# Kernel tuning notes

Measured on AMD Instinct MI355X. Metric: run time of the kernel, lower is better.

Reference implementation:

```python
import jax, jax.numpy as jnp
import numpy as np

N_NODES = 100000
N_EDGES = 3200000
F_IN = 512
F_OUT = 256


def setup_inputs() -> dict:
    key = jax.random.key(0)
    k1, k2, k3, k4, k5 = jax.random.split(key, 5)
    x = jax.random.normal(k1, (N_NODES, F_IN), dtype=jnp.float32)
    adj_rows = jax.random.randint(k2, (N_EDGES,), 0, N_NODES, dtype=jnp.int32)
    adj_cols = jax.random.randint(k3, (N_EDGES,), 0, N_NODES, dtype=jnp.int32)
    adj_vals = jax.random.uniform(k4, (N_EDGES,), dtype=jnp.float32)
    # glorot-uniform weight as in glorot_init
    init_range = np.sqrt(6.0 / (F_IN + F_OUT))
    weight = jax.random.uniform(k5, (F_IN, F_OUT), dtype=jnp.float32,
                                minval=-init_range, maxval=init_range)
    return {"x": x, "adj_rows": adj_rows, "adj_cols": adj_cols,
            "adj_vals": adj_vals, "weight": weight}


def reference(x, adj_rows, adj_cols, adj_vals, adj_rows_dummy=None, **_):
    raise NotImplementedError  # replaced below


def reference(x, adj_rows, adj_cols, adj_vals, weight):
    # dropout p=0.0 -> identity
    h = jnp.matmul(x, weight)                      # [N, Fout] dense GEMM
    # SpMM: out[r] = sum_e vals[e] * h[cols[e]] for rows[e]==r
    msgs = adj_vals[:, None] * h[adj_cols]         # [E, Fout] gather + scale
    out = jax.ops.segment_sum(msgs, adj_rows, num_segments=x.shape[0])
    return jax.nn.relu(out)
```

## Files before the change

kernel.cpp:

```cpp
#include <hip/hip_runtime.h>

#define F_IN 512
#define F_OUT 256
#define BM 128
#define BN 256
#define BK 64

#define RB_BITS 7
#define RPB 128
#define NBUCK 1024
#define NSUB 8
#define CAP_SUB 1024
#define LDSCAP 5120
#define CSTR 16

typedef __attribute__((ext_vector_type(8))) short bf16x8;
typedef __attribute__((ext_vector_type(4))) float f32x4;
typedef __attribute__((ext_vector_type(4))) int i32x4;

__device__ __forceinline__ ushort f2bf(float f) {
    union { float f; unsigned u; } c{f};
    unsigned r = (c.u + 0x7FFF + ((c.u >> 16) & 1)) >> 16;
    return (ushort)r;
}
__device__ __forceinline__ float bf2f(ushort b) {
    union { unsigned u; float f; } c{(unsigned)b << 16};
    return c.f;
}

__global__ __launch_bounds__(256) void conv_w(const float* __restrict__ w,
                                              ushort* __restrict__ wt) {
    int idx = blockIdx.x * 256 + threadIdx.x;
    int k = idx & (F_IN - 1);
    int n = idx >> 9;
    wt[(size_t)n * F_IN + k] = f2bf(w[(size_t)k * F_OUT + n]);
}

__global__ __launch_bounds__(512) void gemm_mfma(const float* __restrict__ x,
                                                 const ushort* __restrict__ wt,
                                                 ushort* __restrict__ h,
                                                 int n_nodes) {
    __shared__ short As[BM * BK];
    __shared__ short Bs[BN * BK];
    const int t = threadIdx.x;
    const int lane = t & 63;
    const int w = t >> 6;
    const int wm = w >> 2;
    const int wn = w & 3;
    const int row0 = blockIdx.x * BM;

    f32x4 acc[4][4] = {};

    const int arow = t >> 2;
    const int akq  = (t & 3) << 4;
    const bool avalid = (row0 + arow) < n_nodes;
    const float* xsrc = x + (size_t)(row0 + arow) * F_IN + akq;

    const int lrow = lane & 15;
    const int koff = (lane >> 4) << 3;

    f32x4 fA[4];
    bf16x8 fB[4];

    {
        if (avalid) {
            const f32x4* s4 = reinterpret_cast<const f32x4*>(xsrc);
            fA[0] = __builtin_nontemporal_load(s4 + 0);
            fA[1] = __builtin_nontemporal_load(s4 + 1);
            fA[2] = __builtin_nontemporal_load(s4 + 2);
            fA[3] = __builtin_nontemporal_load(s4 + 3);
        } else {
            fA[0] = 0.f; fA[1] = 0.f; fA[2] = 0.f; fA[3] = 0.f;
        }
#pragma unroll
        for (int p = 0; p < 4; ++p) {
            int cid = p * 512 + t;
            int n = cid >> 3;
            int j = cid & 7;
            fB[p] = *reinterpret_cast<const bf16x8*>(wt + (size_t)n * F_IN + j * 8);
        }
    }

    for (int k0 = 0; k0 < F_IN; k0 += BK) {
#pragma unroll
        for (int q = 0; q < 2; ++q) {
            bf16x8 v;
#pragma unroll
            for (int j = 0; j < 8; ++j) v[j] = (short)f2bf(fA[q * 2 + (j >> 2)][j & 3]);
            int kk = akq + q * 8;
            int idx = arow * BK + (kk ^ ((arow & 7) << 3));
            *reinterpret_cast<bf16x8*>(&As[idx]) = v;
        }
#pragma unroll
        for (int p = 0; p < 4; ++p) {
            int cid = p * 512 + t;
            int n = cid >> 3;
            int j = cid & 7;
            int idx = n * BK + ((j * 8) ^ ((n & 7) << 3));
            *reinterpret_cast<bf16x8*>(&Bs[idx]) = fB[p];
        }
        __syncthreads();

        if (k0 + BK < F_IN) {
            if (avalid) {
                const f32x4* s4 = reinterpret_cast<const f32x4*>(xsrc + k0 + BK);
                fA[0] = __builtin_nontemporal_load(s4 + 0);
                fA[1] = __builtin_nontemporal_load(s4 + 1);
                fA[2] = __builtin_nontemporal_load(s4 + 2);
                fA[3] = __builtin_nontemporal_load(s4 + 3);
            }
#pragma unroll
            for (int p = 0; p < 4; ++p) {
                int cid = p * 512 + t;
                int n = cid >> 3;
                int j = cid & 7;
                fB[p] = *reinterpret_cast<const bf16x8*>(wt + (size_t)n * F_IN + k0 + BK + j * 8);
            }
        }

#pragma unroll
        for (int kk = 0; kk < BK; kk += 32) {
            bf16x8 a[4], b[4];
#pragma unroll
            for (int m = 0; m < 4; ++m) {
                int r = wm * 64 + m * 16 + lrow;
                int idx = r * BK + ((kk + koff) ^ ((r & 7) << 3));
                a[m] = *reinterpret_cast<const bf16x8*>(&As[idx]);
            }
#pragma unroll
            for (int n = 0; n < 4; ++n) {
                int r = wn * 64 + n * 16 + lrow;
                int idx = r * BK + ((kk + koff) ^ ((r & 7) << 3));
                b[n] = *reinterpret_cast<const bf16x8*>(&Bs[idx]);
            }
#pragma unroll
            for (int m = 0; m < 4; ++m)
#pragma unroll
                for (int n = 0; n < 4; ++n)
                    acc[m][n] = __builtin_amdgcn_mfma_f32_16x16x32_bf16(a[m], b[n], acc[m][n], 0, 0, 0);
        }
        __syncthreads();
    }

    const int rbase = (lane >> 4) << 2;
#pragma unroll
    for (int m = 0; m < 4; ++m) {
#pragma unroll
        for (int r = 0; r < 4; ++r) {
            int orow = row0 + wm * 64 + m * 16 + rbase + r;
            if (orow < n_nodes) {
                ushort* dst = h + (size_t)orow * F_OUT + wn * 64 + lrow;
#pragma unroll
                for (int n = 0; n < 4; ++n) dst[n * 16] = f2bf(acc[m][n][r]);
            }
        }
    }
}

__global__ __launch_bounds__(256) void bucket_place(const int* __restrict__ rows,
                                                    const int* __restrict__ cols,
                                                    const float* __restrict__ vals,
                                                    int* __restrict__ bcur,
                                                    int2* __restrict__ edges,
                                                    int n_edges) {
    const int sub = blockIdx.x & (NSUB - 1);
    int base = (blockIdx.x * 256 + threadIdx.x) * 4;
    if (base >= n_edges) return;
    if (base + 3 < n_edges) {
        i32x4 r4 = __builtin_nontemporal_load(reinterpret_cast<const i32x4*>(rows + base));
        i32x4 c4 = __builtin_nontemporal_load(reinterpret_cast<const i32x4*>(cols + base));
        f32x4 v4 = __builtin_nontemporal_load(reinterpret_cast<const f32x4*>(vals + base));
#pragma unroll
        for (int j = 0; j < 4; ++j) {
            int r = r4[j];
            int bs = (r >> RB_BITS) * NSUB + sub;
            int p = atomicAdd(&bcur[bs * CSTR], 1);
            if (p < CAP_SUB)
                edges[(size_t)bs * CAP_SUB + p] =
                    make_int2(((r & (RPB - 1)) << 17) | c4[j], __float_as_int(v4[j]));
        }
    } else {
        for (int j = 0; j < 4 && base + j < n_edges; ++j) {
            int r = rows[base + j];
            int bs = (r >> RB_BITS) * NSUB + sub;
            int p = atomicAdd(&bcur[bs * CSTR], 1);
            if (p < CAP_SUB)
                edges[(size_t)bs * CAP_SUB + p] =
                    make_int2(((r & (RPB - 1)) << 17) | cols[base + j],
                              __float_as_int(vals[base + j]));
        }
    }
}

__global__ __launch_bounds__(256) void bucket_sort(const int* __restrict__ bcur,
                                                   int2* __restrict__ edges,
                                                   int* __restrict__ offs,
                                                   int* __restrict__ oend,
                                                   int n_nodes) {
    __shared__ int2 raw[LDSCAP];
    __shared__ int cnt[RPB];
    __shared__ int lcur[RPB];
    __shared__ int wtot;
    const int b = blockIdx.x;
    const int t = threadIdx.x;
    const size_t bbase = (size_t)b * NSUB * CAP_SUB;

    if (t < RPB) cnt[t] = 0;
    __syncthreads();

    int nraw = 0;
#pragma unroll
    for (int s = 0; s < NSUB; ++s) {
        int ns = bcur[(b * NSUB + s) * CSTR];
        if (ns > CAP_SUB) ns = CAP_SUB;
        int take = ns;
        if (nraw + take > LDSCAP) take = LDSCAP - nraw;
        for (int i = t; i < take; i += 256) {
            int2 e = edges[bbase + (size_t)s * CAP_SUB + i];
            raw[nraw + i] = e;
            atomicAdd(&cnt[e.x >> 17], 1);
        }
        nraw += take;
    }
    __syncthreads();

    int c = (t < RPB) ? cnt[t] : 0;
    int padded = (c + 7) & ~7;
    int x = padded;
#pragma unroll
    for (int d = 1; d < 64; d <<= 1) {
        int y = __shfl_up(x, d, 64);
        if ((t & 63) >= d) x += y;
    }
    if (t == 63) wtot = x;
    __syncthreads();
    if (t < RPB) {
        int mybase = x - padded + ((t >= 64) ? wtot : 0);
        lcur[t] = mybase;
        int gr = (b << RB_BITS) + t;
        if (gr < n_nodes) {
            offs[gr] = (int)bbase + mybase;
            oend[gr] = (int)bbase + mybase + padded;
        }
        for (int j = c; j < padded; ++j)
            edges[bbase + mybase + j] = make_int2(0, 0);
    }
    __syncthreads();

    for (int i = t; i < nraw; i += 256) {
        int2 e = raw[i];
        int r7 = e.x >> 17;
        int pos = atomicAdd(&lcur[r7], 1);
        edges[bbase + pos] = make_int2(e.x & 0x1FFFF, e.y);
    }
}

struct EB { i32x4 e0, e1, e2, e3; };
struct GB { ushort4 g0, g1, g2, g3, g4, g5, g6, g7; };

__device__ __forceinline__ void load_eb(EB& e, const int2* __restrict__ edges, int i) {
    const i32x4* ep = reinterpret_cast<const i32x4*>(edges + i);
    e.e0 = __builtin_nontemporal_load(ep + 0);
    e.e1 = __builtin_nontemporal_load(ep + 1);
    e.e2 = __builtin_nontemporal_load(ep + 2);
    e.e3 = __builtin_nontemporal_load(ep + 3);
}
__device__ __forceinline__ void issue_gb(GB& g, const EB& e, const ushort* __restrict__ hf) {
    g.g0 = *reinterpret_cast<const ushort4*>(hf + (size_t)e.e0[0] * F_OUT);
    g.g1 = *reinterpret_cast<const ushort4*>(hf + (size_t)e.e0[2] * F_OUT);
    g.g2 = *reinterpret_cast<const ushort4*>(hf + (size_t)e.e1[0] * F_OUT);
    g.g3 = *reinterpret_cast<const ushort4*>(hf + (size_t)e.e1[2] * F_OUT);
    g.g4 = *reinterpret_cast<const ushort4*>(hf + (size_t)e.e2[0] * F_OUT);
    g.g5 = *reinterpret_cast<const ushort4*>(hf + (size_t)e.e2[2] * F_OUT);
    g.g6 = *reinterpret_cast<const ushort4*>(hf + (size_t)e.e3[0] * F_OUT);
    g.g7 = *reinterpret_cast<const ushort4*>(hf + (size_t)e.e3[2] * F_OUT);
}
__device__ __forceinline__ void fma1(float* acc, float v, ushort4 g) {
    acc[0] = fmaf(v, bf2f(g.x), acc[0]);
    acc[1] = fmaf(v, bf2f(g.y), acc[1]);
    acc[2] = fmaf(v, bf2f(g.z), acc[2]);
    acc[3] = fmaf(v, bf2f(g.w), acc[3]);
}
__device__ __forceinline__ void fma_gb(float* acc, const EB& e, const GB& g) {
    fma1(acc, __int_as_float(e.e0[1]), g.g0);
    fma1(acc, __int_as_float(e.e0[3]), g.g1);
    fma1(acc, __int_as_float(e.e1[1]), g.g2);
    fma1(acc, __int_as_float(e.e1[3]), g.g3);
    fma1(acc, __int_as_float(e.e2[1]), g.g4);
    fma1(acc, __int_as_float(e.e2[3]), g.g5);
    fma1(acc, __int_as_float(e.e3[1]), g.g6);
    fma1(acc, __int_as_float(e.e3[3]), g.g7);
}

__global__ __launch_bounds__(256) void spmm_csr(const int* __restrict__ offs,
                                                const int* __restrict__ oend,
                                                const int2* __restrict__ edges,
                                                const ushort* __restrict__ h,
                                                float* __restrict__ out,
                                                int n_nodes) {
    const int row = (int)((blockIdx.x * blockDim.x + threadIdx.x) >> 6);
    if (row >= n_nodes) return;
    const int lane = threadIdx.x & 63;
    const int beg = offs[row];
    const int end = oend[row];
    const int nb = (end - beg) >> 3;

    float acc[4] = {0.f, 0.f, 0.f, 0.f};
    const ushort* hf = h + lane * 4;

    if (nb > 0) {
        EB ea, eb_;
        GB ga, gb;
        load_eb(ea, edges, beg);
        issue_gb(ga, ea, hf);
        int bi = 1;
        for (; bi + 1 < nb; bi += 2) {
            load_eb(eb_, edges, beg + bi * 8);
            issue_gb(gb, eb_, hf);
            fma_gb(acc, ea, ga);
            load_eb(ea, edges, beg + (bi + 1) * 8);
            issue_gb(ga, ea, hf);
            fma_gb(acc, eb_, gb);
        }
        if (bi < nb) {
            load_eb(eb_, edges, beg + bi * 8);
            issue_gb(gb, eb_, hf);
            fma_gb(acc, ea, ga);
            fma_gb(acc, eb_, gb);
        } else {
            fma_gb(acc, ea, ga);
        }
    }

    f32x4 o;
    o[0] = fmaxf(acc[0], 0.f);
    o[1] = fmaxf(acc[1], 0.f);
    o[2] = fmaxf(acc[2], 0.f);
    o[3] = fmaxf(acc[3], 0.f);
    __builtin_nontemporal_store(o, reinterpret_cast<f32x4*>(out + (size_t)row * F_OUT + lane * 4));
}

static inline size_t align_up(size_t v, size_t a) { return (v + a - 1) & ~(a - 1); }

extern "C" void kernel_launch(void* const* d_in, const int* in_sizes, int n_in,
                              void* d_out, int out_size, void* d_ws, size_t ws_size,
                              hipStream_t stream) {
    const float* x    = (const float*)d_in[0];
    const int*   rows = (const int*)d_in[1];
    const int*   cols = (const int*)d_in[2];
    const float* vals = (const float*)d_in[3];
    const float* w    = (const float*)d_in[4];
    float* out = (float*)d_out;

    const int n_nodes = in_sizes[0] / F_IN;
    const int n_edges = in_sizes[1];
    const int nbuck_used = (n_nodes + RPB - 1) >> RB_BITS;

    char* ws = (char*)d_ws;
    size_t off = 0;
    ushort* h   = (ushort*)(ws + off); off = align_up(off + (size_t)n_nodes * F_OUT * 2, 256);
    ushort* wt  = (ushort*)(ws + off); off = align_up(off + (size_t)F_OUT * F_IN * 2, 256);
    int2* edges = (int2*)(ws + off);   off = align_up(off + (size_t)NBUCK * NSUB * CAP_SUB * 8, 256);
    int* offs   = (int*)(ws + off);    off = align_up(off + (size_t)n_nodes * 4, 256);
    int* oend   = (int*)(ws + off);    off = align_up(off + (size_t)n_nodes * 4, 256);
    int* bcur   = (int*)(ws + off);    off = align_up(off + (size_t)NBUCK * NSUB * CSTR * 4, 256);
    (void)ws_size;

    conv_w<<<(F_IN * F_OUT) / 256, 256, 0, stream>>>(w, wt);

    gemm_mfma<<<(n_nodes + BM - 1) / BM, 512, 0, stream>>>(x, wt, h, n_nodes);

    hipMemsetAsync(bcur, 0, (size_t)NBUCK * NSUB * CSTR * 4, stream);
    bucket_place<<<(n_edges / 4 + 255) / 256, 256, 0, stream>>>(rows, cols, vals, bcur,
                                                                edges, n_edges);
    bucket_sort<<<nbuck_used, 256, 0, stream>>>(bcur, edges, offs, oend, n_nodes);

    spmm_csr<<<(n_nodes * 64 + 255) / 256, 256, 0, stream>>>(offs, oend, edges, h, out, n_nodes);
}
```

Baseline: 513.5 us.

## Fuse GEMM and edge bucketing into one launch; sub-sort edges by column

```diff
diff --git a/kernel.cpp b/kernel.cpp
--- a/kernel.cpp
+++ b/kernel.cpp
@@ -13,6 +13,7 @@
 #define CAP_SUB 1024
 #define LDSCAP 5120
 #define CSTR 16
+#define NBIN (RPB * 32)
 
 typedef __attribute__((ext_vector_type(8))) short bf16x8;
 typedef __attribute__((ext_vector_type(4))) float f32x4;
@@ -36,18 +37,61 @@
     wt[(size_t)n * F_IN + k] = f2bf(w[(size_t)k * F_OUT + n]);
 }
 
-__global__ __launch_bounds__(512) void gemm_mfma(const float* __restrict__ x,
-                                                 const ushort* __restrict__ wt,
-                                                 ushort* __restrict__ h,
-                                                 int n_nodes) {
+__global__ __launch_bounds__(512) void gemm_place(const float* __restrict__ x,
+                                                  const ushort* __restrict__ wt,
+                                                  ushort* __restrict__ h,
+                                                  int n_nodes,
+                                                  const int* __restrict__ rows,
+                                                  const int* __restrict__ cols,
+                                                  const float* __restrict__ vals,
+                                                  int* __restrict__ bcur,
+                                                  int2* __restrict__ edges,
+                                                  int n_edges,
+                                                  int ngemm) {
     __shared__ short As[BM * BK];
     __shared__ short Bs[BN * BK];
+    const int bid = blockIdx.x;
     const int t = threadIdx.x;
+
+    const bool is_gemm = (bid % 3 == 0) && (bid / 3 < ngemm);
+    if (!is_gemm) {
+        const int place_id = (bid < 3 * ngemm) ? (bid - bid / 3 - 1) : (bid - ngemm);
+        const int sub = bid & (NSUB - 1);
+        int base = (place_id * 512 + t) * 4;
+        if (base >= n_edges) return;
+        if (base + 3 < n_edges) {
+            i32x4 r4 = __builtin_nontemporal_load(reinterpret_cast<const i32x4*>(rows + base));
+            i32x4 c4 = __builtin_nontemporal_load(reinterpret_cast<const i32x4*>(cols + base));
+            f32x4 v4 = __builtin_nontemporal_load(reinterpret_cast<const f32x4*>(vals + base));
+#pragma unroll
+            for (int j = 0; j < 4; ++j) {
+                int r = r4[j];
+                int bs = (r >> RB_BITS) * NSUB + sub;
+                int p = atomicAdd(&bcur[bs * CSTR], 1);
+                if (p < CAP_SUB)
+                    edges[(size_t)bs * CAP_SUB + p] =
+                        make_int2(((r & (RPB - 1)) << 17) | c4[j], __float_as_int(v4[j]));
+            }
+        } else {
+            for (int j = 0; j < 4 && base + j < n_edges; ++j) {
+                int r = rows[base + j];
+                int bs = (r >> RB_BITS) * NSUB + sub;
+                int p = atomicAdd(&bcur[bs * CSTR], 1);
+                if (p < CAP_SUB)
+                    edges[(size_t)bs * CAP_SUB + p] =
+                        make_int2(((r & (RPB - 1)) << 17) | cols[base + j],
+                                  __float_as_int(vals[base + j]));
+            }
+        }
+        return;
+    }
+
+    const int gb = bid / 3;
     const int lane = t & 63;
     const int w = t >> 6;
     const int wm = w >> 2;
     const int wn = w & 3;
-    const int row0 = blockIdx.x * BM;
+    const int row0 = gb * BM;
 
     f32x4 acc[4][4] = {};
 
@@ -157,55 +201,19 @@
     }
 }
 
-__global__ __launch_bounds__(256) void bucket_place(const int* __restrict__ rows,
-                                                    const int* __restrict__ cols,
-                                                    const float* __restrict__ vals,
-                                                    int* __restrict__ bcur,
-                                                    int2* __restrict__ edges,
-                                                    int n_edges) {
-    const int sub = blockIdx.x & (NSUB - 1);
-    int base = (blockIdx.x * 256 + threadIdx.x) * 4;
-    if (base >= n_edges) return;
-    if (base + 3 < n_edges) {
-        i32x4 r4 = __builtin_nontemporal_load(reinterpret_cast<const i32x4*>(rows + base));
-        i32x4 c4 = __builtin_nontemporal_load(reinterpret_cast<const i32x4*>(cols + base));
-        f32x4 v4 = __builtin_nontemporal_load(reinterpret_cast<const f32x4*>(vals + base));
-#pragma unroll
-        for (int j = 0; j < 4; ++j) {
-            int r = r4[j];
-            int bs = (r >> RB_BITS) * NSUB + sub;
-            int p = atomicAdd(&bcur[bs * CSTR], 1);
-            if (p < CAP_SUB)
-                edges[(size_t)bs * CAP_SUB + p] =
-                    make_int2(((r & (RPB - 1)) << 17) | c4[j], __float_as_int(v4[j]));
-        }
-    } else {
-        for (int j = 0; j < 4 && base + j < n_edges; ++j) {
-            int r = rows[base + j];
-            int bs = (r >> RB_BITS) * NSUB + sub;
-            int p = atomicAdd(&bcur[bs * CSTR], 1);
-            if (p < CAP_SUB)
-                edges[(size_t)bs * CAP_SUB + p] =
-                    make_int2(((r & (RPB - 1)) << 17) | cols[base + j],
-                              __float_as_int(vals[base + j]));
-        }
-    }
-}
-
 __global__ __launch_bounds__(256) void bucket_sort(const int* __restrict__ bcur,
                                                    int2* __restrict__ edges,
                                                    int* __restrict__ offs,
                                                    int* __restrict__ oend,
                                                    int n_nodes) {
     __shared__ int2 raw[LDSCAP];
-    __shared__ int cnt[RPB];
-    __shared__ int lcur[RPB];
+    __shared__ int cnt[NBIN];
     __shared__ int wtot;
     const int b = blockIdx.x;
     const int t = threadIdx.x;
     const size_t bbase = (size_t)b * NSUB * CAP_SUB;
 
-    if (t < RPB) cnt[t] = 0;
+    for (int i = t; i < NBIN; i += 256) cnt[i] = 0;
     __syncthreads();
 
     int nraw = 0;
@@ -218,14 +226,19 @@
         for (int i = t; i < take; i += 256) {
             int2 e = edges[bbase + (size_t)s * CAP_SUB + i];
             raw[nraw + i] = e;
-            atomicAdd(&cnt[e.x >> 17], 1);
+            int key = ((e.x >> 17) << 5) | ((e.x & 0x1FFFF) >> 12);
+            atomicAdd(&cnt[key], 1);
         }
         nraw += take;
     }
     __syncthreads();
 
-    int c = (t < RPB) ? cnt[t] : 0;
-    int padded = (c + 7) & ~7;
+    int rowtot = 0;
+    if (t < RPB) {
+#pragma unroll
+        for (int j = 0; j < 32; ++j) rowtot += cnt[(t << 5) + j];
+    }
+    int padded = (rowtot + 7) & ~7;
     int x = padded;
 #pragma unroll
     for (int d = 1; d < 64; d <<= 1) {
@@ -235,22 +248,28 @@
     if (t == 63) wtot = x;
     __syncthreads();
     if (t < RPB) {
-        int mybase = x - padded + ((t >= 64) ? wtot : 0);
-        lcur[t] = mybase;
+        int rb = x - padded + ((t >= 64) ? wtot : 0);
         int gr = (b << RB_BITS) + t;
         if (gr < n_nodes) {
-            offs[gr] = (int)bbase + mybase;
-            oend[gr] = (int)bbase + mybase + padded;
-        }
-        for (int j = c; j < padded; ++j)
-            edges[bbase + mybase + j] = make_int2(0, 0);
+            offs[gr] = (int)bbase + rb;
+            oend[gr] = (int)bbase + rb + padded;
+        }
+        for (int j = rowtot; j < padded; ++j)
+            edges[bbase + rb + j] = make_int2(0, 0);
+        int run = rb;
+#pragma unroll
+        for (int j = 0; j < 32; ++j) {
+            int c2 = cnt[(t << 5) + j];
+            cnt[(t << 5) + j] = run;
+            run += c2;
+        }
     }
     __syncthreads();
 
     for (int i = t; i < nraw; i += 256) {
         int2 e = raw[i];
-        int r7 = e.x >> 17;
-        int pos = atomicAdd(&lcur[r7], 1);
+        int key = ((e.x >> 17) << 5) | ((e.x & 0x1FFFF) >> 12);
+        int pos = atomicAdd(&cnt[key], 1);
         edges[bbase + pos] = make_int2(e.x & 0x1FFFF, e.y);
     }
 }
@@ -367,12 +386,14 @@
     (void)ws_size;
 
     conv_w<<<(F_IN * F_OUT) / 256, 256, 0, stream>>>(w, wt);
-
-    gemm_mfma<<<(n_nodes + BM - 1) / BM, 512, 0, stream>>>(x, wt, h, n_nodes);
-
     hipMemsetAsync(bcur, 0, (size_t)NBUCK * NSUB * CSTR * 4, stream);
-    bucket_place<<<(n_edges / 4 + 255) / 256, 256, 0, stream>>>(rows, cols, vals, bcur,
-                                                                edges, n_edges);
+
+    const int ngemm  = (n_nodes + BM - 1) / BM;
+    const int nplace = (n_edges + 2047) / 2048;
+    gemm_place<<<ngemm + nplace, 512, 0, stream>>>(x, wt, h, n_nodes,
+                                                   rows, cols, vals, bcur, edges,
+                                                   n_edges, ngemm);
+
     bucket_sort<<<nbuck_used, 256, 0, stream>>>(bcur, edges, offs, oend, n_nodes);
 
     spmm_csr<<<(n_nodes * 64 + 255) / 256, 256, 0, stream>>>(offs, oend, edges, h, out, n_nodes);
```

Result: faster. 448.9 us (-12.6%).
